# Performance work log

Hardware: AMD Instinct MI355X
Metric: run time of the kernel (lower is better)

Reference implementation:

```python
import jax, jax.numpy as jnp
import numpy as np

N_AGENTS = 32
UNIT_DIM = 32
STATE_DIM = 1200
N_HEAD = 8
EMBED = 64
KEY_HID = 2 * EMBED
HYPER = 256
V_HID = 4 * EMBED
ATTEND_REG_COEF = 0.001
BS, T = 128, 32


def setup_inputs() -> dict:
    key = jax.random.key(0)
    ks = jax.random.split(key, 12)
    def lin(k, shape, fan_in):
        return jax.random.normal(k, shape, jnp.float32) / np.sqrt(fan_in)
    return dict(
        agent_qs=jax.random.normal(ks[0], (BS, T, N_AGENTS), jnp.float32),
        states=jax.random.normal(ks[1], (BS, T, STATE_DIM), jnp.float32),
        actions=jax.random.randint(ks[2], (BS, T, N_AGENTS), 0, 20),
        sel_W1=lin(ks[3], (N_HEAD, HYPER, STATE_DIM), STATE_DIM),
        sel_b1=jnp.zeros((N_HEAD, HYPER), jnp.float32),
        sel_W2=lin(ks[4], (N_HEAD, EMBED, HYPER), HYPER),
        key_W1=lin(ks[5], (N_HEAD, KEY_HID, UNIT_DIM + 1), UNIT_DIM + 1),
        key_b1=jnp.zeros((N_HEAD, KEY_HID), jnp.float32),
        key_W2=lin(ks[6], (N_HEAD, EMBED, KEY_HID), KEY_HID),
        wh_W1=lin(ks[7], (HYPER, STATE_DIM), STATE_DIM),
        wh_b1=jnp.zeros((HYPER,), jnp.float32),
        wh_W2=lin(ks[8], (N_HEAD, HYPER), HYPER),
        wh_b2=jnp.zeros((N_HEAD,), jnp.float32),
        v_W1=lin(ks[9], (V_HID, STATE_DIM), STATE_DIM),
        v_b1=jnp.zeros((V_HID,), jnp.float32),
        v_W2=lin(ks[10], (1, V_HID), V_HID),
        v_b2=jnp.zeros((1,), jnp.float32),
    )


def reference(agent_qs, states, actions, sel_W1, sel_b1, sel_W2, key_W1, key_b1, key_W2,
              wh_W1, wh_b1, wh_W2, wh_b2, v_W1, v_b1, v_W2, v_b2):
    bs = agent_qs.shape[0]
    s = states.reshape(-1, STATE_DIM)                       # (B, S), B = bs*T
    B = s.shape[0]
    units = s[:, :UNIT_DIM * N_AGENTS].reshape(B, N_AGENTS, UNIT_DIM)  # (B, A, U)
    q = agent_qs.reshape(B, N_AGENTS)                       # (B, A)
    # nonlinear=True: append each agent's q to its unit features
    units = jnp.concatenate([units, q[:, :, None]], axis=2)  # (B, A, U+1)
    a = actions.reshape(B, N_AGENTS)
    # selector hypernets (all heads batched): (B, H, E)
    h1 = jax.nn.relu(jnp.einsum('bs,hes->bhe', s, sel_W1) + sel_b1[None])
    sel = jnp.einsum('bhe,hde->bhd', h1, sel_W2)
    # key hypernets (all heads x all agents batched): (B, H, A, E)
    k1 = jax.nn.relu(jnp.einsum('bau,hku->bhak', units, key_W1) + key_b1[None, :, None, :])
    keys = jnp.einsum('bhak,hdk->bhad', k1, key_W2)
    logits = jnp.einsum('bhd,bhad->bha', sel, keys)          # unscaled, used for regularizer
    scaled = logits / np.sqrt(EMBED)
    scaled = jnp.where(a[:, None, :] == 0, -99999999.0, scaled)  # mask_dead
    w = jax.nn.softmax(scaled, axis=2)                       # (B, H, A)
    head_q = jnp.einsum('ba,bha->bh', q, w)                  # (B, H)
    # weighted_head + state_bias
    wh = jnp.abs(jax.nn.relu(s @ wh_W1.T + wh_b1) @ wh_W2.T + wh_b2)  # (B, H)
    v = (jax.nn.relu(s @ v_W1.T + v_b1) @ v_W2.T + v_b2)[:, 0]        # (B,)
    y = (wh * head_q).sum(axis=1) + v
    q_tot = y.reshape(bs, -1, 1)
    # sum over heads of per-head mean of squared (unscaled) logits
    attend_mag_regs = ATTEND_REG_COEF * (logits ** 2).mean(axis=(0, 2)).sum()
    # per-head entropy: sum over agents, mean over batch
    head_entropies = -(jnp.log(w + 1e-8) * w).sum(axis=2).mean(axis=0)  # (H,)
    return q_tot, attend_mag_regs, head_entropies
```

## Files before the change

kernel.cpp:

```cpp
#include <hip/hip_runtime.h>

#define B_TOT 4096
#define SDIM  1200
#define KPAD  1216
#define NA    32
#define NH    8
#define EMB   64
#define KHID  128
#define HYP   256
#define NSEL  2048
#define NTOT  2560

#define WS_H1BF 0
#define WS_MBF  (WS_H1BF + (size_t)B_TOT * NTOT / 2)
#define WS_LG   (WS_MBF  + (size_t)B_TOT * NH * KHID / 2)
#define WS_PART (WS_LG   + (size_t)B_TOT * NH * NA)
#define WS_P2   (WS_PART + (size_t)B_TOT * 16)
#define WS_ABF  (WS_P2   + (size_t)32 * 16)
#define WS_WBF  (WS_ABF  + (size_t)B_TOT * KPAD / 2)
#define WS_KW32 (WS_WBF  + (size_t)NTOT * KPAD / 2)
#define WS_W32F (WS_KW32 + (size_t)1024 * 32 / 2)
#define WS_M2T  (WS_W32F + (size_t)1024)

#define CVT_A_BLK 4864
#define CVT_W_BLK 3040

typedef __attribute__((ext_vector_type(8))) short short8v;
typedef __attribute__((ext_vector_type(4))) float floatx4;

#define GLL16(gsrc, ldst) __builtin_amdgcn_global_load_lds( \
    (const __attribute__((address_space(1))) unsigned int*)(gsrc), \
    (__attribute__((address_space(3))) unsigned int*)(ldst), 16, 0, 0)

__device__ __forceinline__ ushort f2bf(float x) {
    unsigned u = __builtin_bit_cast(unsigned, x);
    unsigned r = (u + 0x7FFFu + ((u >> 16) & 1u)) >> 16;
    return (ushort)r;
}
__device__ __forceinline__ float bf2f(ushort u) {
    unsigned x = ((unsigned)u) << 16;
    return __builtin_bit_cast(float, x);
}

__global__ __launch_bounds__(256) void k_cvt_all(
    const float* __restrict__ states, const float* __restrict__ sel_W1,
    const float* __restrict__ wh_W1, const float* __restrict__ v_W1,
    const float* __restrict__ key_W1, ushort* __restrict__ Abf,
    ushort* __restrict__ Wbf, ushort* __restrict__ kw32,
    float* __restrict__ w32f)
{
    const int gb = blockIdx.x;
    if (gb < CVT_A_BLK) {
        const size_t g = (size_t)gb * 256 + threadIdx.x;
        const int row = (int)(g / (KPAD / 4));
        const int c4  = (int)(g % (KPAD / 4)) * 4;
        ushort4 o = {0, 0, 0, 0};
        if (c4 < SDIM) {
            float4 v = *(const float4*)(states + (size_t)row * SDIM + c4);
            o.x = f2bf(v.x); o.y = f2bf(v.y); o.z = f2bf(v.z); o.w = f2bf(v.w);
        }
        *(ushort4*)(Abf + (size_t)row * KPAD + c4) = o;
    } else if (gb < CVT_A_BLK + CVT_W_BLK) {
        const size_t g = (size_t)(gb - CVT_A_BLK) * 256 + threadIdx.x;
        const int row = (int)(g / (KPAD / 4));
        const int c4  = (int)(g % (KPAD / 4)) * 4;
        const float* src = (row < NSEL)       ? (sel_W1 + (size_t)row * SDIM)
                         : (row < NSEL + HYP) ? (wh_W1 + (size_t)(row - NSEL) * SDIM)
                                              : (v_W1  + (size_t)(row - NSEL - HYP) * SDIM);
        ushort4 o = {0, 0, 0, 0};
        if (c4 < SDIM) {
            float4 v = *(const float4*)(src + c4);
            o.x = f2bf(v.x); o.y = f2bf(v.y); o.z = f2bf(v.z); o.w = f2bf(v.w);
        }
        *(ushort4*)(Wbf + (size_t)row * KPAD + c4) = o;
    } else {
        const int row = (gb - CVT_A_BLK - CVT_W_BLK) * 256 + threadIdx.x;
        if (row >= 1024) return;
        const float* srcr = key_W1 + (size_t)row * 33;
        ushort o[32];
        #pragma unroll
        for (int u = 0; u < 32; ++u) o[u] = f2bf(srcr[u]);
        #pragma unroll
        for (int c = 0; c < 4; ++c)
            *(short8v*)(kw32 + (size_t)row * 32 + c * 8) = *(short8v*)&o[c * 8];
        w32f[row] = srcr[32];
    }
}

__global__ __launch_bounds__(256) void k_m2(
    const float* __restrict__ sel_W2, const float* __restrict__ key_W2,
    ushort* __restrict__ M2T)
{
    __shared__ float ssel[EMB * HYP];
    __shared__ float skey[EMB][8];
    const int t  = threadIdx.x;
    const int h  = blockIdx.x;
    const int k0 = blockIdx.y * 8;

    const float4* sw = (const float4*)(sel_W2 + (size_t)h * EMB * HYP);
    #pragma unroll
    for (int j = 0; j < 16; ++j)
        ((float4*)ssel)[j * 256 + t] = sw[j * 256 + t];
    if (t < EMB) {
        #pragma unroll
        for (int kk = 0; kk < 8; ++kk)
            skey[t][kk] = key_W2[((size_t)h * EMB + t) * KHID + k0 + kk];
    }
    __syncthreads();

    const int e = t;
    float acc[8] = {};
    for (int d = 0; d < EMB; ++d) {
        const float sv = ssel[d * HYP + e];
        #pragma unroll
        for (int kk = 0; kk < 8; ++kk)
            acc[kk] = fmaf(sv, skey[d][kk], acc[kk]);
    }
    #pragma unroll
    for (int kk = 0; kk < 8; ++kk)
        M2T[((size_t)h * KHID + k0 + kk) * HYP + e] = f2bf(acc[kk]);
}

#define BKG 64
__global__ __launch_bounds__(256) void k_gemm1_mfma(
    const ushort* __restrict__ Abf, const ushort* __restrict__ Wbf,
    const float* __restrict__ sel_b1, const float* __restrict__ wh_b1,
    const float* __restrict__ v_b1, ushort* __restrict__ h1bf)
{
    __shared__ ushort As[128 * BKG];
    __shared__ ushort Bs[128 * BKG];
    const int tid = threadIdx.x;
    const int l   = tid & 63;
    const int w   = tid >> 6;
    const int wM  = w >> 1, wN = w & 1;
    const int arow0 = blockIdx.y * 128;
    const int nrow0 = blockIdx.x * 128;

    const int srow   = tid >> 3;
    const int schunk = tid & 7;
    const int scol   = (schunk ^ (srow & 7)) * 8;
    const ushort* gA = Abf + (size_t)(arow0 + srow) * KPAD + scol;
    const ushort* gB = Wbf + (size_t)(nrow0 + srow) * KPAD + scol;
    ushort* lA = &As[tid * 8];
    ushort* lB = &Bs[tid * 8];

    floatx4 acc[4][4] = {};

    for (int k0 = 0; k0 < KPAD; k0 += BKG) {
        #pragma unroll
        for (int c = 0; c < 4; ++c) {
            GLL16(gA + (size_t)(c * 32) * KPAD + k0, lA + c * 2048);
            GLL16(gB + (size_t)(c * 32) * KPAD + k0, lB + c * 2048);
        }
        __syncthreads();

        #pragma unroll
        for (int kk = 0; kk < 2; ++kk) {
            const int ch = kk * 4 + (l >> 4);
            short8v av[4], bv[4];
            #pragma unroll
            for (int mi = 0; mi < 4; ++mi) {
                const int row = wM * 64 + mi * 16 + (l & 15);
                av[mi] = *(const short8v*)&As[row * BKG + (ch ^ (row & 7)) * 8];
            }
            #pragma unroll
            for (int ni = 0; ni < 4; ++ni) {
                const int row = wN * 64 + ni * 16 + (l & 15);
                bv[ni] = *(const short8v*)&Bs[row * BKG + (ch ^ (row & 7)) * 8];
            }
            #pragma unroll
            for (int mi = 0; mi < 4; ++mi)
                #pragma unroll
                for (int ni = 0; ni < 4; ++ni)
                    acc[mi][ni] = __builtin_amdgcn_mfma_f32_16x16x32_bf16(
                        av[mi], bv[ni], acc[mi][ni], 0, 0, 0);
        }
        __syncthreads();
    }

    float bias_n[4];
    #pragma unroll
    for (int ni = 0; ni < 4; ++ni) {
        const int col = nrow0 + wN * 64 + ni * 16 + (l & 15);
        bias_n[ni] = (col < NSEL)       ? sel_b1[col]
                   : (col < NSEL + HYP) ? wh_b1[col - NSEL]
                                        : v_b1[col - NSEL - HYP];
    }
    #pragma unroll
    for (int mi = 0; mi < 4; ++mi) {
        const int row = arow0 + wM * 64 + mi * 16 + (l >> 4) * 4;
        #pragma unroll
        for (int ni = 0; ni < 4; ++ni) {
            const int col = nrow0 + wN * 64 + ni * 16 + (l & 15);
            #pragma unroll
            for (int r = 0; r < 4; ++r)
                h1bf[(size_t)(row + r) * NTOT + col] =
                    f2bf(fmaxf(acc[mi][ni][r] + bias_n[ni], 0.f));
        }
    }
}

#define BK 32
__global__ __launch_bounds__(256) void k_m_mfma(
    const ushort* __restrict__ h1bf, const ushort* __restrict__ M2T,
    ushort* __restrict__ m_out)
{
    __shared__ ushort As[2][64 * BK];
    __shared__ ushort Bs[2][128 * BK];
    const int tid = threadIdx.x;
    const int l   = tid & 63;
    const int w   = tid >> 6;
    const int wM  = w >> 1, wN = w & 1;
    const int h     = blockIdx.x;
    const int brow0 = blockIdx.y * 64;

    const int srow = tid >> 2;
    const int skof = (tid & 3) * 8;
    const ushort* gA = h1bf + (size_t)(brow0 + srow) * NTOT + h * HYP + skof;
    const ushort* gB = M2T + ((size_t)h * KHID + srow) * HYP + skof;

#define STAGE_M(BUF, KK) do { \
    GLL16(gA + (KK), &As[BUF][srow * BK + skof]); \
    GLL16(gB + (KK), &Bs[BUF][srow * BK + skof]); \
    GLL16(gB + (size_t)64 * HYP + (KK), &Bs[BUF][(64 + srow) * BK + skof]); \
} while (0)

    floatx4 acc[2][4] = {};

    STAGE_M(0, 0);
    __syncthreads();
    int cur = 0;
    for (int k0 = 0; k0 < HYP; k0 += BK) {
        if (k0 + BK < HYP) STAGE_M(cur ^ 1, k0 + BK);

        const int kch = (l >> 4) * 8;
        short8v av[2], bv[4];
        #pragma unroll
        for (int mi = 0; mi < 2; ++mi)
            av[mi] = *(const short8v*)&As[cur][(wM * 32 + mi * 16 + (l & 15)) * BK + kch];
        #pragma unroll
        for (int ni = 0; ni < 4; ++ni)
            bv[ni] = *(const short8v*)&Bs[cur][(wN * 64 + ni * 16 + (l & 15)) * BK + kch];
        #pragma unroll
        for (int mi = 0; mi < 2; ++mi)
            #pragma unroll
            for (int ni = 0; ni < 4; ++ni)
                acc[mi][ni] = __builtin_amdgcn_mfma_f32_16x16x32_bf16(
                    av[mi], bv[ni], acc[mi][ni], 0, 0, 0);
        __syncthreads();
        cur ^= 1;
    }

    #pragma unroll
    for (int mi = 0; mi < 2; ++mi) {
        const int row = brow0 + wM * 32 + mi * 16 + (l >> 4) * 4;
        #pragma unroll
        for (int ni = 0; ni < 4; ++ni) {
            const int col = wN * 64 + ni * 16 + (l & 15);
            #pragma unroll
            for (int r = 0; r < 4; ++r)
                m_out[((size_t)(row + r) * NH + h) * KHID + col] =
                    f2bf(acc[mi][ni][r]);
        }
    }
}

__global__ __launch_bounds__(256) void k_logits_mfma(
    const ushort* __restrict__ Abf, const ushort* __restrict__ KW32,
    const float* __restrict__ W32f, const float* __restrict__ key_b1,
    const float* __restrict__ agent_qs, const ushort* __restrict__ m_in,
    float* __restrict__ logits)
{
    const int tid = threadIdx.x;
    const int l   = tid & 63;
    const int w   = tid >> 6;
    const int wid = blockIdx.x * 4 + w;
    const int b   = wid >> 1;
    const int h0  = (wid & 1) * 4;

    short8v av[2];
    float4 qv[2];
    #pragma unroll
    for (int mi = 0; mi < 2; ++mi) {
        const int a = mi * 16 + (l & 15);
        av[mi] = *(const short8v*)(
            Abf + (size_t)b * KPAD + a * 32 + (l >> 4) * 8);
        qv[mi] = *(const float4*)(
            agent_qs + (size_t)b * NA + mi * 16 + (l >> 4) * 4);
    }

    #pragma unroll
    for (int hh = 0; hh < 4; ++hh) {
        const int h = h0 + hh;
        short8v bv[8];
        float b1r[8], w32r[8], mr[8];
        #pragma unroll
        for (int ni = 0; ni < 8; ++ni) {
            const int k = ni * 16 + (l & 15);
            bv[ni]   = *(const short8v*)(
                KW32 + ((size_t)h * KHID + k) * 32 + (l >> 4) * 8);
            b1r[ni]  = key_b1[h * KHID + k];
            w32r[ni] = W32f[h * KHID + k];
            mr[ni]   = bf2f(m_in[((size_t)b * NH + h) * KHID + k]);
        }
        floatx4 acc[2][8] = {};
        #pragma unroll
        for (int mi = 0; mi < 2; ++mi)
            #pragma unroll
            for (int ni = 0; ni < 8; ++ni)
                acc[mi][ni] = __builtin_amdgcn_mfma_f32_16x16x32_bf16(
                    av[mi], bv[ni], acc[mi][ni], 0, 0, 0);

        #pragma unroll
        for (int mi = 0; mi < 2; ++mi) {
            float s0 = 0.f, s1 = 0.f, s2 = 0.f, s3 = 0.f;
            #pragma unroll
            for (int ni = 0; ni < 8; ++ni) {
                const float b1v = b1r[ni], wv = w32r[ni], mv = mr[ni];
                s0 = fmaf(fmaxf(fmaf(qv[mi].x, wv, acc[mi][ni][0] + b1v), 0.f), mv, s0);
                s1 = fmaf(fmaxf(fmaf(qv[mi].y, wv, acc[mi][ni][1] + b1v), 0.f), mv, s1);
                s2 = fmaf(fmaxf(fmaf(qv[mi].z, wv, acc[mi][ni][2] + b1v), 0.f), mv, s2);
                s3 = fmaf(fmaxf(fmaf(qv[mi].w, wv, acc[mi][ni][3] + b1v), 0.f), mv, s3);
            }
            #pragma unroll
            for (int off = 8; off >= 1; off >>= 1) {
                s0 += __shfl_xor(s0, off);
                s1 += __shfl_xor(s1, off);
                s2 += __shfl_xor(s2, off);
                s3 += __shfl_xor(s3, off);
            }
            if ((l & 15) == 0) {
                float4 o = {s0, s1, s2, s3};
                *(float4*)(logits + ((size_t)b * NH + h) * NA
                           + mi * 16 + (l >> 4) * 4) = o;
            }
        }
    }
}

__global__ __launch_bounds__(256) void k_softmax(
    const float* __restrict__ logits, const float* __restrict__ agent_qs,
    const int* __restrict__ actions, const ushort* __restrict__ h1bf,
    const float* __restrict__ wh_W2, const float* __restrict__ wh_b2,
    const float* __restrict__ v_W2, const float* __restrict__ v_b2,
    float* __restrict__ out, float* __restrict__ part)
{
    __shared__ float qs[NA];
    __shared__ int   act_s[NA];
    __shared__ float whs[NH];
    __shared__ float hq[NH];
    __shared__ float vred[4];
    const int b = blockIdx.x, t = threadIdx.x;
    if (t < NA) {
        qs[t]    = agent_qs[(size_t)b * NA + t];
        act_s[t] = actions[(size_t)b * NA + t];
    }
    const int h = t >> 5, a = t & 31;
    {
        float acc = 0.f;
        #pragma unroll
        for (int j = 0; j < 8; ++j) {
            const int e = a + 32 * j;
            acc = fmaf(bf2f(h1bf[(size_t)b * NTOT + NSEL + e]),
                       wh_W2[h * HYP + e], acc);
        }
        #pragma unroll
        for (int off = 16; off >= 1; off >>= 1) acc += __shfl_xor(acc, off, 32);
        if (a == 0) whs[h] = fabsf(acc + wh_b2[h]);
    }
    {
        float acc = bf2f(h1bf[(size_t)b * NTOT + NSEL + HYP + t]) * v_W2[t];
        #pragma unroll
        for (int off = 32; off >= 1; off >>= 1) acc += __shfl_xor(acc, off);
        if ((t & 63) == 0) vred[t >> 6] = acc;
    }
    __syncthreads();

    const float lg = logits[((size_t)b * NH + h) * NA + a];
    float sc = (act_s[a] == 0) ? -99999999.0f : lg * 0.125f;

    float mx = sc;
    #pragma unroll
    for (int off = 16; off >= 1; off >>= 1) mx = fmaxf(mx, __shfl_xor(mx, off, 32));
    const float e = expf(sc - mx);
    float sum = e;
    #pragma unroll
    for (int off = 16; off >= 1; off >>= 1) sum += __shfl_xor(sum, off, 32);
    const float wgt = e / sum;

    float r_sq  = lg * lg;
    float r_hq  = qs[a] * wgt;
    float r_ent = -wgt * logf(wgt + 1e-8f);
    #pragma unroll
    for (int off = 16; off >= 1; off >>= 1) {
        r_sq  += __shfl_xor(r_sq,  off, 32);
        r_hq  += __shfl_xor(r_hq,  off, 32);
        r_ent += __shfl_xor(r_ent, off, 32);
    }
    if (a == 0) {
        hq[h] = r_hq;
        part[(size_t)b * 16 + h]     = r_sq;
        part[(size_t)b * 16 + 8 + h] = r_ent;
    }
    __syncthreads();
    if (t == 0) {
        float y = vred[0] + vred[1] + vred[2] + vred[3] + v_b2[0];
        #pragma unroll
        for (int i = 0; i < NH; ++i) y = fmaf(whs[i], hq[i], y);
        out[b] = y;
    }
}

__global__ __launch_bounds__(256) void k_final_s1(
    const float* __restrict__ part, float* __restrict__ part2)
{
    __shared__ float red[16][17];
    const int t = threadIdx.x;
    const int c = t & 15, rl = t >> 4;
    const int rbase = blockIdx.x * 128 + rl;
    float v0 = 0.f, v1 = 0.f, v2 = 0.f, v3 = 0.f;
    #pragma unroll
    for (int j = 0; j < 8; j += 4) {
        v0 += part[(size_t)(rbase + (j + 0) * 16) * 16 + c];
        v1 += part[(size_t)(rbase + (j + 1) * 16) * 16 + c];
        v2 += part[(size_t)(rbase + (j + 2) * 16) * 16 + c];
        v3 += part[(size_t)(rbase + (j + 3) * 16) * 16 + c];
    }
    red[rl][c] = (v0 + v1) + (v2 + v3);
    __syncthreads();
    if (t < 16) {
        float s = 0.f;
        #pragma unroll
        for (int i = 0; i < 16; ++i) s += red[i][t];
        part2[blockIdx.x * 16 + t] = s;
    }
}

__global__ __launch_bounds__(256) void k_final_s2(
    const float* __restrict__ part2, float* __restrict__ out)
{
    __shared__ float red[16][17];
    __shared__ float tot[16];
    const int t = threadIdx.x;
    {
        const int g = t >> 4, c = t & 15;
        red[g][c] = part2[t] + part2[t + 256];
    }
    __syncthreads();
    if (t < 16) {
        float s = 0.f;
        #pragma unroll
        for (int i = 0; i < 16; ++i) s += red[i][t];
        tot[t] = s;
    }
    __syncthreads();
    if (t == 0) {
        float s = 0.f;
        #pragma unroll
        for (int i = 0; i < 8; ++i) s += tot[i];
        out[B_TOT] = 0.001f * (s / (float)((size_t)B_TOT * NA));
    }
    if (t >= 8 && t < 16)
        out[B_TOT + 1 + (t - 8)] = tot[t] / (float)B_TOT;
}

extern "C" void kernel_launch(void* const* d_in, const int* in_sizes, int n_in,
                              void* d_out, int out_size, void* d_ws, size_t ws_size,
                              hipStream_t stream) {
    (void)in_sizes; (void)n_in; (void)out_size; (void)ws_size;
    const float* agent_qs = (const float*)d_in[0];
    const float* states   = (const float*)d_in[1];
    const int*   actions  = (const int*)d_in[2];
    const float* sel_W1   = (const float*)d_in[3];
    const float* sel_b1   = (const float*)d_in[4];
    const float* sel_W2   = (const float*)d_in[5];
    const float* key_W1   = (const float*)d_in[6];
    const float* key_b1   = (const float*)d_in[7];
    const float* key_W2   = (const float*)d_in[8];
    const float* wh_W1    = (const float*)d_in[9];
    const float* wh_b1    = (const float*)d_in[10];
    const float* wh_W2    = (const float*)d_in[11];
    const float* wh_b2    = (const float*)d_in[12];
    const float* v_W1     = (const float*)d_in[13];
    const float* v_b1     = (const float*)d_in[14];
    const float* v_W2     = (const float*)d_in[15];
    const float* v_b2     = (const float*)d_in[16];

    float* out = (float*)d_out;
    float* ws  = (float*)d_ws;
    ushort* h1bf  = (ushort*)(ws + WS_H1BF);
    ushort* m_buf = (ushort*)(ws + WS_MBF);
    float* lg_buf = ws + WS_LG;
    float* part   = ws + WS_PART;
    float* part2  = ws + WS_P2;
    ushort* Abf   = (ushort*)(ws + WS_ABF);
    ushort* Wbf   = (ushort*)(ws + WS_WBF);
    ushort* KW32  = (ushort*)(ws + WS_KW32);
    float*  W32f  = ws + WS_W32F;
    ushort* M2T   = (ushort*)(ws + WS_M2T);

    k_cvt_all<<<CVT_A_BLK + CVT_W_BLK + 4, 256, 0, stream>>>(
        states, sel_W1, wh_W1, v_W1, key_W1, Abf, Wbf, KW32, W32f);
    k_m2<<<dim3(NH, KHID / 8), 256, 0, stream>>>(sel_W2, key_W2, M2T);
    k_gemm1_mfma<<<dim3(NTOT / 128, B_TOT / 128), 256, 0, stream>>>(
        Abf, Wbf, sel_b1, wh_b1, v_b1, h1bf);
    k_m_mfma<<<dim3(NH, B_TOT / 64), 256, 0, stream>>>(h1bf, M2T, m_buf);
    k_logits_mfma<<<dim3(B_TOT / 2), 256, 0, stream>>>(
        Abf, KW32, W32f, key_b1, agent_qs, m_buf, lg_buf);
    k_softmax<<<dim3(B_TOT), 256, 0, stream>>>(
        lg_buf, agent_qs, actions, h1bf, wh_W2, wh_b2, v_W2, v_b2, out, part);
    k_final_s1<<<32, 256, 0, stream>>>(part, part2);
    k_final_s2<<<1, 256, 0, stream>>>(part2, out);
}
```

Measured before the change: 115.2 us.

## Repack m and key bias/w32 into lane-contiguous bf16 layouts for logits kernel

The m output of k_m_mfma is stored in a permuted layout so each lane of the logits kernel fetches its 8 m values with one 16-byte load instead of 8 scalar loads. The key_W1 q-column weight and key_b1 are packed together as bf16 pairs in the same lane-friendly order, replacing four separate float gathers. The logits kernel also adds an occupancy hint through launch_bounds, disables unrolling of the head loop, and raises wave priority around the MFMA block. Storing the bias and weight in bf16 instead of fp32 lowers their precision slightly.

```diff
diff --git a/kernel.cpp b/kernel.cpp
--- a/kernel.cpp
+++ b/kernel.cpp
@@ -19,8 +19,8 @@
 #define WS_ABF  (WS_P2   + (size_t)32 * 16)
 #define WS_WBF  (WS_ABF  + (size_t)B_TOT * KPAD / 2)
 #define WS_KW32 (WS_WBF  + (size_t)NTOT * KPAD / 2)
-#define WS_W32F (WS_KW32 + (size_t)1024 * 32 / 2)
-#define WS_M2T  (WS_W32F + (size_t)1024)
+#define WS_B2P  (WS_KW32 + (size_t)1024 * 32 / 2)
+#define WS_M2T  (WS_B2P  + (size_t)2048 / 2)
 
 #define CVT_A_BLK 4864
 #define CVT_W_BLK 3040
@@ -45,9 +45,9 @@
 __global__ __launch_bounds__(256) void k_cvt_all(
     const float* __restrict__ states, const float* __restrict__ sel_W1,
     const float* __restrict__ wh_W1, const float* __restrict__ v_W1,
-    const float* __restrict__ key_W1, ushort* __restrict__ Abf,
-    ushort* __restrict__ Wbf, ushort* __restrict__ kw32,
-    float* __restrict__ w32f)
+    const float* __restrict__ key_W1, const float* __restrict__ key_b1,
+    ushort* __restrict__ Abf, ushort* __restrict__ Wbf,
+    ushort* __restrict__ kw32, ushort* __restrict__ b2p)
 {
     const int gb = blockIdx.x;
     if (gb < CVT_A_BLK) {
@@ -83,7 +83,10 @@
         #pragma unroll
         for (int c = 0; c < 4; ++c)
             *(short8v*)(kw32 + (size_t)row * 32 + c * 8) = *(short8v*)&o[c * 8];
-        w32f[row] = srcr[32];
+        const int h = row >> 7, k = row & 127;
+        const size_t po = (((size_t)h * 16 + (k & 15)) * 8 + (k >> 4)) * 2;
+        b2p[po]     = f2bf(srcr[32]);
+        b2p[po + 1] = f2bf(key_b1[row]);
     }
 }
 
@@ -259,17 +262,16 @@
             const int col = wN * 64 + ni * 16 + (l & 15);
             #pragma unroll
             for (int r = 0; r < 4; ++r)
-                m_out[((size_t)(row + r) * NH + h) * KHID + col] =
-                    f2bf(acc[mi][ni][r]);
-        }
-    }
-}
-
-__global__ __launch_bounds__(256) void k_logits_mfma(
+                m_out[(((size_t)(row + r) * NH + h) * 16 + (col & 15)) * 8 + (col >> 4)]
+                    = f2bf(acc[mi][ni][r]);
+        }
+    }
+}
+
+__global__ __launch_bounds__(256, 5) void k_logits_mfma(
     const ushort* __restrict__ Abf, const ushort* __restrict__ KW32,
-    const float* __restrict__ W32f, const float* __restrict__ key_b1,
-    const float* __restrict__ agent_qs, const ushort* __restrict__ m_in,
-    float* __restrict__ logits)
+    const ushort* __restrict__ B2p, const float* __restrict__ agent_qs,
+    const ushort* __restrict__ mT, float* __restrict__ logits)
 {
     const int tid = threadIdx.x;
     const int l   = tid & 63;
@@ -289,38 +291,49 @@
             agent_qs + (size_t)b * NA + mi * 16 + (l >> 4) * 4);
     }
 
-    #pragma unroll
+    #pragma clang loop unroll(disable)
     for (int hh = 0; hh < 4; ++hh) {
         const int h = h0 + hh;
+        const int bpo = (h * 16 + (l & 15)) * 16;
+        short8v wb0 = *(const short8v*)&B2p[bpo];
+        short8v wb1 = *(const short8v*)&B2p[bpo + 8];
         short8v bv[8];
-        float b1r[8], w32r[8], mr[8];
         #pragma unroll
         for (int ni = 0; ni < 8; ++ni) {
             const int k = ni * 16 + (l & 15);
-            bv[ni]   = *(const short8v*)(
+            bv[ni] = *(const short8v*)(
                 KW32 + ((size_t)h * KHID + k) * 32 + (l >> 4) * 8);
-            b1r[ni]  = key_b1[h * KHID + k];
-            w32r[ni] = W32f[h * KHID + k];
-            mr[ni]   = bf2f(m_in[((size_t)b * NH + h) * KHID + k]);
-        }
+        }
+        short8v mv = *(const short8v*)(
+            mT + (((size_t)b * NH + h) * 16 + (l & 15)) * 8);
+        float mr[8], w32r[8], b1r[8];
+        #pragma unroll
+        for (int ni = 0; ni < 8; ++ni) {
+            mr[ni]   = bf2f((ushort)mv[ni]);
+            w32r[ni] = bf2f((ushort)((ni < 4) ? wb0[ni * 2]       : wb1[(ni - 4) * 2]));
+            b1r[ni]  = bf2f((ushort)((ni < 4) ? wb0[ni * 2 + 1]   : wb1[(ni - 4) * 2 + 1]));
+        }
+
         floatx4 acc[2][8] = {};
+        __builtin_amdgcn_s_setprio(1);
         #pragma unroll
         for (int mi = 0; mi < 2; ++mi)
             #pragma unroll
             for (int ni = 0; ni < 8; ++ni)
                 acc[mi][ni] = __builtin_amdgcn_mfma_f32_16x16x32_bf16(
                     av[mi], bv[ni], acc[mi][ni], 0, 0, 0);
+        __builtin_amdgcn_s_setprio(0);
 
         #pragma unroll
         for (int mi = 0; mi < 2; ++mi) {
             float s0 = 0.f, s1 = 0.f, s2 = 0.f, s3 = 0.f;
             #pragma unroll
             for (int ni = 0; ni < 8; ++ni) {
-                const float b1v = b1r[ni], wv = w32r[ni], mv = mr[ni];
-                s0 = fmaf(fmaxf(fmaf(qv[mi].x, wv, acc[mi][ni][0] + b1v), 0.f), mv, s0);
-                s1 = fmaf(fmaxf(fmaf(qv[mi].y, wv, acc[mi][ni][1] + b1v), 0.f), mv, s1);
-                s2 = fmaf(fmaxf(fmaf(qv[mi].z, wv, acc[mi][ni][2] + b1v), 0.f), mv, s2);
-                s3 = fmaf(fmaxf(fmaf(qv[mi].w, wv, acc[mi][ni][3] + b1v), 0.f), mv, s3);
+                const float b1v = b1r[ni], wv = w32r[ni], mv2 = mr[ni];
+                s0 = fmaf(fmaxf(fmaf(qv[mi].x, wv, acc[mi][ni][0] + b1v), 0.f), mv2, s0);
+                s1 = fmaf(fmaxf(fmaf(qv[mi].y, wv, acc[mi][ni][1] + b1v), 0.f), mv2, s1);
+                s2 = fmaf(fmaxf(fmaf(qv[mi].z, wv, acc[mi][ni][2] + b1v), 0.f), mv2, s2);
+                s3 = fmaf(fmaxf(fmaf(qv[mi].w, wv, acc[mi][ni][3] + b1v), 0.f), mv2, s3);
             }
             #pragma unroll
             for (int off = 8; off >= 1; off >>= 1) {
@@ -496,17 +509,17 @@
     ushort* Abf   = (ushort*)(ws + WS_ABF);
     ushort* Wbf   = (ushort*)(ws + WS_WBF);
     ushort* KW32  = (ushort*)(ws + WS_KW32);
-    float*  W32f  = ws + WS_W32F;
+    ushort* B2p   = (ushort*)(ws + WS_B2P);
     ushort* M2T   = (ushort*)(ws + WS_M2T);
 
     k_cvt_all<<<CVT_A_BLK + CVT_W_BLK + 4, 256, 0, stream>>>(
-        states, sel_W1, wh_W1, v_W1, key_W1, Abf, Wbf, KW32, W32f);
+        states, sel_W1, wh_W1, v_W1, key_W1, key_b1, Abf, Wbf, KW32, B2p);
     k_m2<<<dim3(NH, KHID / 8), 256, 0, stream>>>(sel_W2, key_W2, M2T);
     k_gemm1_mfma<<<dim3(NTOT / 128, B_TOT / 128), 256, 0, stream>>>(
         Abf, Wbf, sel_b1, wh_b1, v_b1, h1bf);
     k_m_mfma<<<dim3(NH, B_TOT / 64), 256, 0, stream>>>(h1bf, M2T, m_buf);
     k_logits_mfma<<<dim3(B_TOT / 2), 256, 0, stream>>>(
-        Abf, KW32, W32f, key_b1, agent_qs, m_buf, lg_buf);
+        Abf, KW32, B2p, agent_qs, m_buf, lg_buf);
     k_softmax<<<dim3(B_TOT), 256, 0, stream>>>(
         lg_buf, agent_qs, actions, h1bf, wh_W2, wh_b2, v_W2, v_b2, out, part);
     k_final_s1<<<32, 256, 0, stream>>>(part, part2);
```

After: 151.5 us. +31.5%, slower.
